# Kernel optimization log

Measured on AMD Instinct MI355X. Metric: run time of the kernel, lower is better.

Reference implementation:

```python
import jax, jax.numpy as jnp
import numpy as np

H, W = 960, 1920
NLAYERS, NSUB = 16, 2
L = NLAYERS * NSUB
DMIN, DMAX = 2.0, 20.0
SIG_OFF = 5.0
N_RAYS = 65536


def setup_inputs() -> dict:
    key = jax.random.key(0)
    k1, k2, k3, k4 = jax.random.split(key, 4)
    origins = jax.random.normal(k1, (N_RAYS, 3), jnp.float32) * 0.1  # inside innermost sphere (r=2)
    d = jax.random.normal(k2, (N_RAYS, 3), jnp.float32)
    directions = d / jnp.linalg.norm(d, axis=-1, keepdims=True)
    alpha = jax.random.uniform(k3, (L, 1, H, W), jnp.float32, -1.0, 1.0)
    rgb = jax.random.uniform(k4, (NLAYERS, 3, H, W), jnp.float32, -1.0, 1.0)
    planes_init = 1.0 / np.linspace(1.0 / DMIN, 1.0 / DMAX, L)
    layer_deltas = jnp.asarray(np.log(np.diff(planes_init)), jnp.float32)
    center = jnp.zeros((3,), jnp.float32)
    return dict(origins=origins, directions=directions, alpha=alpha, rgb=rgb,
                layer_deltas=layer_deltas, center=center)


def _bilinear(plane, gx, gy):
    # plane: (C,H,W); gx,gy: (N,) normalized coords in [-1,1]; align_corners=True.
    # Coords are always in-range (points lie on the sphere) so clipping suffices
    # (reflection padding is never exercised).
    C, Hh, Ww = plane.shape
    x = (gx + 1.0) * 0.5 * (Ww - 1)
    y = (gy + 1.0) * 0.5 * (Hh - 1)
    x0f = jnp.floor(x)
    y0f = jnp.floor(y)
    wx = x - x0f
    wy = y - y0f
    x0 = jnp.clip(x0f.astype(jnp.int32), 0, Ww - 1)
    x1 = jnp.clip(x0f.astype(jnp.int32) + 1, 0, Ww - 1)
    y0 = jnp.clip(y0f.astype(jnp.int32), 0, Hh - 1)
    y1 = jnp.clip(y0f.astype(jnp.int32) + 1, 0, Hh - 1)
    v00 = plane[:, y0, x0]
    v01 = plane[:, y0, x1]
    v10 = plane[:, y1, x0]
    v11 = plane[:, y1, x1]
    return v00 * (1 - wx) * (1 - wy) + v01 * wx * (1 - wy) + v10 * (1 - wx) * wy + v11 * wx * wy


_sample = jax.vmap(_bilinear, in_axes=(0, 0, 0))  # per-layer plane lookup


def _forward(origins, directions, alpha, rgb, layer_deltas, center):
    # radii of concentric spheres (cumsum recovers planes_init exactly)
    radii = jnp.cumsum(jnp.concatenate([jnp.array([DMIN], jnp.float32), jnp.exp(layer_deltas)]))  # (L,)
    O = origins[:, None, :]      # (N,1,3)
    D = directions[:, None, :]   # (N,1,3)
    ray = O - center
    a = jnp.sum(D * D, axis=-1)                 # (N,1) -> broadcasts to (N,L)
    b = 2.0 * jnp.sum(D * ray, axis=-1)
    c = jnp.sum(ray * ray, axis=-1) - radii[None] ** 2
    disc = b * b - 4.0 * a * c
    sq = jnp.sqrt(jnp.maximum(disc, 0.0))
    t0 = (-b + sq) / (2.0 * a)                  # (N,L)
    t1 = (-b - sq) / (2.0 * a)
    mask = (t0 * t1) < 0                        # origin inside sphere -> (N,L)
    inter = O + D * t0[..., None]               # (N,L,3)
    xyzn = (inter - center) / radii[None, :, None]
    gx = xyzn[..., 2].T                                          # (L,N) width coord = z
    gy = (jnp.arctan2(xyzn[..., 1], -xyzn[..., 0]) / jnp.pi).T   # (L,N) height coord = azimuth
    alphas = _sample(alpha, gx, gy)[:, 0, :]                     # (L,N)
    alphas = jax.nn.sigmoid(alphas - SIG_OFF) * mask.T.astype(alphas.dtype)
    rgbs = jax.nn.sigmoid(_sample(rgb, gx[::NSUB], gy[::NSUB]))  # (nlayers,3,N)
    rgbs = jnp.repeat(rgbs, NSUB, axis=0)                        # (L,3,N)
    # front-to-back alpha composite over increasing radius
    trans = jnp.cumprod(1.0 - alphas, axis=0)
    trans = jnp.concatenate([jnp.ones((1, alphas.shape[1]), alphas.dtype), trans[:-1]], axis=0)
    weights = alphas * trans                                     # (L,N)
    out = jnp.einsum('ln,lcn->nc', weights, rgbs)                # (N,3)
    return out


def reference(origins, directions, alpha, rgb, layer_deltas, center):
    return _forward(origins, directions, alpha, rgb, layer_deltas, center)
```

## Files before the change

kernel.cpp:

```cpp
#include <hip/hip_runtime.h>
#include <math.h>

#define HH 960
#define WW 1920
#define LTOT 32
#define HWSZ (HH * WW)
#define NRAYS 65536
#define SIG_OFF_F 5.0f
#define DMIN_F 2.0f

__device__ __forceinline__ float sigmoidf(float x) {
    return 1.0f / (1.0f + expf(-x));
}

__global__ __launch_bounds__(256) void msi_forward(
    const float* __restrict__ origins,
    const float* __restrict__ directions,
    const float* __restrict__ alpha,
    const float* __restrict__ rgb,
    const float* __restrict__ layer_deltas,
    const float* __restrict__ center,
    float* __restrict__ out)
{
    __shared__ float s_radii[LTOT];
    if (threadIdx.x == 0) {
        float r = DMIN_F;
        s_radii[0] = r;
        for (int i = 0; i < LTOT - 1; ++i) {
            r += expf(layer_deltas[i]);
            s_radii[i + 1] = r;
        }
    }
    __syncthreads();

    const int gid  = blockIdx.x * 256 + threadIdx.x;
    const int ray  = gid >> 5;
    const int lane = threadIdx.x & 31;

    const float cx = center[0], cy = center[1], cz = center[2];
    const float ox = origins[ray * 3 + 0];
    const float oy = origins[ray * 3 + 1];
    const float oz = origins[ray * 3 + 2];
    const float dxv = directions[ray * 3 + 0];
    const float dyv = directions[ray * 3 + 1];
    const float dzv = directions[ray * 3 + 2];

    const float rx = ox - cx, ry = oy - cy, rz = oz - cz;
    const float a  = dxv * dxv + dyv * dyv + dzv * dzv;
    const float b  = 2.0f * (dxv * rx + dyv * ry + dzv * rz);
    const float c0 = rx * rx + ry * ry + rz * rz;

    const float r    = s_radii[lane];
    const float c    = c0 - r * r;
    const float disc = b * b - 4.0f * a * c;
    const float sq   = sqrtf(fmaxf(disc, 0.0f));
    const float t0   = (-b + sq) / (2.0f * a);
    const float t1   = (-b - sq) / (2.0f * a);
    const bool  mask = (t0 * t1) < 0.0f;

    const float px = (ox + dxv * t0) - cx;
    const float py = (oy + dyv * t0) - cy;
    const float pz = (oz + dzv * t0) - cz;
    const float nx = px / r, ny = py / r, nz = pz / r;

    const float gx = nz;
    const float gy = atan2f(ny, -nx) * 0.31830988618379067f;

    const float x   = (gx + 1.0f) * 0.5f * (float)(WW - 1);
    const float y   = (gy + 1.0f) * 0.5f * (float)(HH - 1);
    const float x0f = floorf(x), y0f = floorf(y);
    const float wx  = x - x0f,  wy  = y - y0f;
    int ix0 = (int)x0f, iy0 = (int)y0f;
    int ix1 = ix0 + 1,  iy1 = iy0 + 1;
    ix0 = min(max(ix0, 0), WW - 1);
    ix1 = min(max(ix1, 0), WW - 1);
    iy0 = min(max(iy0, 0), HH - 1);
    iy1 = min(max(iy1, 0), HH - 1);

    const float w00 = (1.0f - wx) * (1.0f - wy);
    const float w01 = wx * (1.0f - wy);
    const float w10 = (1.0f - wx) * wy;
    const float w11 = wx * wy;

    const int i00 = iy0 * WW + ix0;
    const int i01 = iy0 * WW + ix1;
    const int i10 = iy1 * WW + ix0;
    const int i11 = iy1 * WW + ix1;

    const float* ap = alpha + (size_t)lane * HWSZ;
    const float sv = ap[i00] * w00 + ap[i01] * w01 + ap[i10] * w10 + ap[i11] * w11;
    float av = sigmoidf(sv - SIG_OFF_F);
    av = mask ? av : 0.0f;

    float cr = 0.0f, cg = 0.0f, cb = 0.0f;
    if ((lane & 1) == 0) {
        const float* rp = rgb + (size_t)(lane >> 1) * 3 * HWSZ;
        {
            const float* q = rp;
            cr = sigmoidf(q[i00] * w00 + q[i01] * w01 + q[i10] * w10 + q[i11] * w11);
        }
        {
            const float* q = rp + HWSZ;
            cg = sigmoidf(q[i00] * w00 + q[i01] * w01 + q[i10] * w10 + q[i11] * w11);
        }
        {
            const float* q = rp + 2 * HWSZ;
            cb = sigmoidf(q[i00] * w00 + q[i01] * w01 + q[i10] * w10 + q[i11] * w11);
        }
    }
    const int src = lane & ~1;
    cr = __shfl(cr, src, 32);
    cg = __shfl(cg, src, 32);
    cb = __shfl(cb, src, 32);

    float p = 1.0f - av;
    #pragma unroll
    for (int off = 1; off < 32; off <<= 1) {
        const float v = __shfl_up(p, off, 32);
        if (lane >= off) p *= v;
    }
    float trans = __shfl_up(p, 1, 32);
    if (lane == 0) trans = 1.0f;
    const float wgt = av * trans;

    float accR = wgt * cr;
    float accG = wgt * cg;
    float accB = wgt * cb;
    #pragma unroll
    for (int off = 16; off >= 1; off >>= 1) {
        accR += __shfl_xor(accR, off, 32);
        accG += __shfl_xor(accG, off, 32);
        accB += __shfl_xor(accB, off, 32);
    }
    if (lane == 0) {
        out[ray * 3 + 0] = accR;
        out[ray * 3 + 1] = accG;
        out[ray * 3 + 2] = accB;
    }
}

extern "C" void kernel_launch(void* const* d_in, const int* in_sizes, int n_in,
                              void* d_out, int out_size, void* d_ws, size_t ws_size,
                              hipStream_t stream) {
    const float* origins      = (const float*)d_in[0];
    const float* directions   = (const float*)d_in[1];
    const float* alpha        = (const float*)d_in[2];
    const float* rgb          = (const float*)d_in[3];
    const float* layer_deltas = (const float*)d_in[4];
    const float* center       = (const float*)d_in[5];
    float* out = (float*)d_out;

    const int total   = NRAYS * LTOT;
    const int threads = 256;
    const int blocks  = total / threads;
    msi_forward<<<blocks, threads, 0, stream>>>(origins, directions, alpha, rgb,
                                                layer_deltas, center, out);
}
```

Before: 688.6 us.

## Sort rays by direction bins to improve texture-gather locality

Adds a counting-sort pass (histogram, scan, scatter) that groups rays into 64x64 bins by the angular coordinate of their direction. The main kernel then processes rays in that permuted order, so neighbouring warps sample nearby texels across all layers and cache hit rates should rise for the scattered bilinear gathers. The cost is three extra small launches, a memset and one indirection load per ray. The bins are keyed on direction alone, which only approximates where each ray lands because the origins are small offsets from the center.

```diff
diff --git a/kernel.cpp b/kernel.cpp
--- a/kernel.cpp
+++ b/kernel.cpp
@@ -9,8 +9,73 @@
 #define SIG_OFF_F 5.0f
 #define DMIN_F 2.0f
 
+#define NBX 64
+#define NBY 64
+#define NBINS (NBX * NBY)
+
 __device__ __forceinline__ float sigmoidf(float x) {
     return 1.0f / (1.0f + expf(-x));
+}
+
+__global__ __launch_bounds__(256) void bin_count(
+    const float* __restrict__ directions,
+    int* __restrict__ keys,
+    int* __restrict__ hist)
+{
+    const int r = blockIdx.x * 256 + threadIdx.x;
+    const float dx = directions[r * 3 + 0];
+    const float dy = directions[r * 3 + 1];
+    const float dz = directions[r * 3 + 2];
+    const float gx = dz;
+    const float gy = atan2f(dy, -dx) * 0.31830988618379067f;
+    int kx = (int)((gx + 1.0f) * 0.5f * (float)NBX);
+    int ky = (int)((gy + 1.0f) * 0.5f * (float)NBY);
+    kx = min(max(kx, 0), NBX - 1);
+    ky = min(max(ky, 0), NBY - 1);
+    const int key = ky * NBX + kx;
+    keys[r] = key;
+    atomicAdd(&hist[key], 1);
+}
+
+__global__ __launch_bounds__(1024) void scan_bins(
+    const int* __restrict__ hist,
+    int* __restrict__ offs)
+{
+    __shared__ int s_wave[16];
+    __shared__ int s_waveoff[16];
+    const int t = threadIdx.x;
+    const int4 v = ((const int4*)hist)[t];
+    const int total = v.x + v.y + v.z + v.w;
+    const int lane = t & 63, wid = t >> 6;
+    int inc = total;
+    #pragma unroll
+    for (int off = 1; off < 64; off <<= 1) {
+        const int u = __shfl_up(inc, off, 64);
+        if (lane >= off) inc += u;
+    }
+    if (lane == 63) s_wave[wid] = inc;
+    __syncthreads();
+    if (t == 0) {
+        int acc = 0;
+        for (int i = 0; i < 16; ++i) { s_waveoff[i] = acc; acc += s_wave[i]; }
+    }
+    __syncthreads();
+    const int excl = s_waveoff[wid] + inc - total;
+    offs[4 * t + 0] = excl;
+    offs[4 * t + 1] = excl + v.x;
+    offs[4 * t + 2] = excl + v.x + v.y;
+    offs[4 * t + 3] = excl + v.x + v.y + v.z;
+}
+
+__global__ __launch_bounds__(256) void scatter_rays(
+    const int* __restrict__ keys,
+    int* __restrict__ offs,
+    int* __restrict__ perm)
+{
+    const int r = blockIdx.x * 256 + threadIdx.x;
+    const int key = keys[r];
+    const int pos = atomicAdd(&offs[key], 1);
+    perm[pos] = r;
 }
 
 __global__ __launch_bounds__(256) void msi_forward(
@@ -20,6 +85,7 @@
     const float* __restrict__ rgb,
     const float* __restrict__ layer_deltas,
     const float* __restrict__ center,
+    const int* __restrict__ perm,
     float* __restrict__ out)
 {
     __shared__ float s_radii[LTOT];
@@ -34,7 +100,7 @@
     __syncthreads();
 
     const int gid  = blockIdx.x * 256 + threadIdx.x;
-    const int ray  = gid >> 5;
+    const int ray  = perm[gid >> 5];
     const int lane = threadIdx.x & 31;
 
     const float cx = center[0], cy = center[1], cz = center[2];
@@ -150,9 +216,18 @@
     const float* center       = (const float*)d_in[5];
     float* out = (float*)d_out;
 
-    const int total   = NRAYS * LTOT;
-    const int threads = 256;
-    const int blocks  = total / threads;
-    msi_forward<<<blocks, threads, 0, stream>>>(origins, directions, alpha, rgb,
-                                                layer_deltas, center, out);
-}
+    char* ws  = (char*)d_ws;
+    int* hist = (int*)(ws);
+    int* offs = (int*)(ws + 16384);
+    int* keys = (int*)(ws + 32768);
+    int* perm = (int*)(ws + 32768 + NRAYS * sizeof(int));
+
+    hipMemsetAsync(hist, 0, NBINS * sizeof(int), stream);
+    bin_count<<<NRAYS / 256, 256, 0, stream>>>(directions, keys, hist);
+    scan_bins<<<1, 1024, 0, stream>>>(hist, offs);
+    scatter_rays<<<NRAYS / 256, 256, 0, stream>>>(keys, offs, perm);
+
+    const int blocks = (NRAYS * LTOT) / 256;
+    msi_forward<<<blocks, 256, 0, stream>>>(origins, directions, alpha, rgb,
+                                            layer_deltas, center, perm, out);
+}
```

Result: faster. 654.8 us (-4.9%).
